# Kernel tuning notes

Measured on AMD Instinct MI355X. Metric: run time of the kernel, lower is better.

The kernel has to match this reference:

```python
import jax, jax.numpy as jnp
import numpy as np


def setup_inputs() -> dict:
    key = jax.random.key(0)
    k1, k2 = jax.random.split(key)
    T, K, D = 100000, 512, 64
    flags_matrix = jax.random.uniform(k1, (T, K), dtype=jnp.float32)  # ~half > 0.5
    emb_weight = jax.random.normal(k2, (K, D), dtype=jnp.float32)
    return {"flags_matrix": flags_matrix, "emb_weight": emb_weight}


def reference(flags_matrix, emb_weight):
    # mask[t,k] = 1 if flag active; bag-of-embeddings mean over active items per row.
    mask = (flags_matrix > 0.5).astype(emb_weight.dtype)          # [T, K]
    counts = jnp.sum(mask, axis=1, keepdims=True)                  # [T, 1]
    sums = mask @ emb_weight                                       # [T, D] masked sum of embeddings
    # rows with no active flags -> zeros (matches the torch branch)
    return jnp.where(counts > 0, sums / jnp.maximum(counts, 1.0), 0.0)
```

## Files before the change

### kernel.cpp

```cpp
#include <hip/hip_runtime.h>
#include <stdint.h>


#define T_ROWS 100000
#define K_FLAGS 512
#define D_DIM 64
#define TILES (T_ROWS / 16)

typedef __attribute__((ext_vector_type(4))) float f32x4;
typedef __attribute__((ext_vector_type(8))) short bf16x8;

__device__ __forceinline__ uint32_t f32_to_bf16_rne(float f) {
  union { float f; uint32_t u; } v; v.f = f;
  uint32_t u = v.u;
  return (u + 0x7FFFu + ((u >> 16) & 1u)) >> 16;
}

__global__ __launch_bounds__(1024, 8) void flagbag_kernel(const float* __restrict__ flags,
                                                          const float* __restrict__ W,
                                                          float* __restrict__ out) {
  __shared__ uint4 sB[16 * 4 * 64];
  __shared__ uint32_t sM[16][256];

  const int tid  = threadIdx.x;
  const int lane = tid & 63;
  const int wave = tid >> 6;
  const int tile = wave * 512 + (int)blockIdx.x;
  const bool active = (tile < TILES);
  const int t0 = (active ? tile : 0) * 16;

  if (active) {
    const float* ft = flags + (size_t)t0 * K_FLAGS + lane * 8;

    uint32_t D0 = 0, D1 = 0, D2 = 0, D3 = 0;
    f32x4 ra[4], rb[4];
#pragma unroll
    for (int r = 0; r < 3; ++r) {
      ra[r] = *reinterpret_cast<const f32x4*>(ft + r * K_FLAGS);
      rb[r] = *reinterpret_cast<const f32x4*>(ft + r * K_FLAGS + 4);
    }
#pragma unroll
    for (int r = 0; r < 16; ++r) {
      if (r + 3 < 16) {
        ra[(r + 3) & 3] = *reinterpret_cast<const f32x4*>(ft + (r + 3) * K_FLAGS);
        rb[(r + 3) & 3] = *reinterpret_cast<const f32x4*>(ft + (r + 3) * K_FLAGS + 4);
      }
      const f32x4 a = ra[r & 3], b = rb[r & 3];
      uint32_t byte = 0;
#pragma unroll
      for (int j = 0; j < 4; ++j) {
        byte |= (a[j] > 0.5f) ? (1u << j)       : 0u;
        byte |= (b[j] > 0.5f) ? (1u << (j + 4)) : 0u;
      }
      const uint32_t sh = byte << ((r & 3) * 8);
      if ((r >> 2) == 0) D0 |= sh;
      else if ((r >> 2) == 1) D1 |= sh;
      else if ((r >> 2) == 2) D2 |= sh;
      else D3 |= sh;
    }

    uint32_t* sMw = sM[wave];
    sMw[0 * 64 + (lane ^ 0)]  = D0;
    sMw[1 * 64 + (lane ^ 4)]  = D1;
    sMw[2 * 64 + (lane ^ 8)]  = D2;
    sMw[3 * 64 + (lane ^ 12)] = D3;
  }

  if (tid < 32) {
    const int e = tid >> 1, h = tid & 1;
    const uint32_t d = (((e >> (2 * h)) & 1)     ? 0x00003F80u : 0u) |
                       (((e >> (2 * h + 1)) & 1) ? 0x3F800000u : 0u);
    sM[15][e * 2 + h] = d;
  }

#pragma unroll
  for (int p = 0; p < 4; ++p) {
    const int E  = tid + p * 1024;
    const int s  = E >> 8;
    const int nt = (E >> 6) & 3;
    const int ln = E & 63;
    const int n  = (ln & 15) + 16 * nt;
    const int kb = 128 * (ln >> 4) + 8 * s;
    uint32_t r[4];
#pragma unroll
    for (int j = 0; j < 4; ++j) {
      uint32_t lo = f32_to_bf16_rne(W[(size_t)(kb + 2 * j    ) * D_DIM + n]);
      uint32_t hi = f32_to_bf16_rne(W[(size_t)(kb + 2 * j + 1) * D_DIM + n]);
      r[j] = lo | (hi << 16);
    }
    sB[E] = make_uint4(r[0], r[1], r[2], r[3]);
  }
  __syncthreads();
  if (!active) return;

  const int m  = lane & 15;
  const int kq = lane >> 4;
  const int mj = m >> 2, mb = m & 3;
  const uint32_t* sMw = sM[wave];
  const uint32_t* lut = sM[15];

  const uint4* sbl = &sB[lane];
  f32x4 acc[4];
#pragma unroll
  for (int nt = 0; nt < 4; ++nt) acc[nt] = (f32x4){0.f, 0.f, 0.f, 0.f};

  uint4 bc[4], bn[4];
#pragma unroll
  for (int nt = 0; nt < 4; ++nt) bc[nt] = sbl[nt * 64];

  int cnt = 0;
#pragma unroll
  for (int g = 0; g < 4; ++g) {
    const uint4 md = *reinterpret_cast<const uint4*>(&sMw[mj * 64 + 16 * kq + 4 * (g ^ mj)]);

#pragma unroll
    for (int q = 0; q < 4; ++q) {
      const int s = 4 * g + q;
      if (s + 1 < 16) {
#pragma unroll
        for (int nt = 0; nt < 4; ++nt) bn[nt] = sbl[((s + 1) * 4 + nt) * 64];
      }
      const uint32_t dw = (q == 0) ? md.x : (q == 1) ? md.y : (q == 2) ? md.z : md.w;
      const uint32_t byte = (dw >> (8 * mb)) & 0xFFu;
      cnt += __popc(byte);

      union { uint32_t d[4]; bf16x8 v; } af;
      const uint2 lo = *reinterpret_cast<const uint2*>(&lut[(byte & 15u) * 2]);
      const uint2 hi = *reinterpret_cast<const uint2*>(&lut[(byte >> 4) * 2]);
      af.d[0] = lo.x; af.d[1] = lo.y; af.d[2] = hi.x; af.d[3] = hi.y;

#pragma unroll
      for (int nt = 0; nt < 4; ++nt)
        acc[nt] = __builtin_amdgcn_mfma_f32_16x16x32_bf16(
            *reinterpret_cast<const bf16x8*>(&bc[nt]), af.v, acc[nt], 0, 0, 0);

#pragma unroll
      for (int nt = 0; nt < 4; ++nt) bc[nt] = bn[nt];
    }
  }

  cnt += __shfl_xor(cnt, 16);
  cnt += __shfl_xor(cnt, 32);
  const float inv = (cnt > 0) ? (1.0f / (float)cnt) : 0.0f;

  float* obase = out + (size_t)(t0 + m) * D_DIM + 4 * kq;
#pragma unroll
  for (int nt = 0; nt < 4; ++nt) {
    f32x4 v;
#pragma unroll
    for (int r = 0; r < 4; ++r) v[r] = acc[nt][r] * inv;
    *reinterpret_cast<f32x4*>(obase + 16 * nt) = v;
  }
}

extern "C" void kernel_launch(void* const* d_in, const int* in_sizes, int n_in,
                              void* d_out, int out_size, void* d_ws, size_t ws_size,
                              hipStream_t stream) {
  const float* flags = (const float*)d_in[0];
  const float* W     = (const float*)d_in[1];
  float* out         = (float*)d_out;

  hipLaunchKernelGGL(flagbag_kernel, dim3(512), dim3(1024), 0, stream, flags, W, out);
}
```

Before: 41.34 us.

## Switch to 32x32x16 MFMA with wave pairs sharing 32-row tiles

Each pair of waves now handles a 32-row tile, and each wave computes half of the 64 output columns using 32x32x16 bf16 MFMAs instead of four 16x16x32 MFMAs per step. Two accumulators alternate across k-steps so that consecutive dependent MFMAs are split, and they are summed at the end. The shared-memory B layout and the mask-byte addressing are rewritten to match the new operand layout. This reduces the number of MFMA issues and B-fragment LDS loads per row. In exchange it adds a per-step byte LDS read, and each wave now depends on its mate wave's mask data.

```diff
diff --git a/kernel.cpp b/kernel.cpp
--- a/kernel.cpp
+++ b/kernel.cpp
@@ -5,10 +5,11 @@
 #define T_ROWS 100000
 #define K_FLAGS 512
 #define D_DIM 64
-#define TILES (T_ROWS / 16)
+#define PAIRS (T_ROWS / 32)
 
-typedef __attribute__((ext_vector_type(4))) float f32x4;
-typedef __attribute__((ext_vector_type(8))) short bf16x8;
+typedef __attribute__((ext_vector_type(4)))  float f32x4;
+typedef __attribute__((ext_vector_type(16))) float f32x16;
+typedef __attribute__((ext_vector_type(8)))  short bf16x8;
 
 __device__ __forceinline__ uint32_t f32_to_bf16_rne(float f) {
   union { float f; uint32_t u; } v; v.f = f;
@@ -19,15 +20,17 @@
 __global__ __launch_bounds__(1024, 8) void flagbag_kernel(const float* __restrict__ flags,
                                                           const float* __restrict__ W,
                                                           float* __restrict__ out) {
-  __shared__ uint4 sB[16 * 4 * 64];
+  __shared__ uint4 sB[32 * 2 * 64];
   __shared__ uint32_t sM[16][256];
 
   const int tid  = threadIdx.x;
   const int lane = tid & 63;
   const int wave = tid >> 6;
-  const int tile = wave * 512 + (int)blockIdx.x;
-  const bool active = (tile < TILES);
-  const int t0 = (active ? tile : 0) * 16;
+  const int mate = wave & 1;
+  const int pair = (wave >> 1) * 512 + (int)blockIdx.x;
+  const bool active = (pair < PAIRS);
+  const int pb = (active ? pair : 0) * 32;
+  const int t0 = pb + 16 * mate;
 
   if (active) {
     const float* ft = flags + (size_t)t0 * K_FLAGS + lane * 8;
@@ -76,11 +79,11 @@
 #pragma unroll
   for (int p = 0; p < 4; ++p) {
     const int E  = tid + p * 1024;
-    const int s  = E >> 8;
-    const int nt = (E >> 6) & 3;
+    const int s  = E >> 7;
+    const int nt = (E >> 6) & 1;
     const int ln = E & 63;
-    const int n  = (ln & 15) + 16 * nt;
-    const int kb = 128 * (ln >> 4) + 8 * s;
+    const int n  = (ln & 31) + 32 * nt;
+    const int kb = 16 * s + 8 * (ln >> 5);
     uint32_t r[4];
 #pragma unroll
     for (int j = 0; j < 4; ++j) {
@@ -93,63 +96,52 @@
   __syncthreads();
   if (!active) return;
 
-  const int m  = lane & 15;
-  const int kq = lane >> 4;
-  const int mj = m >> 2, mb = m & 3;
-  const uint32_t* sMw = sM[wave];
+  const int trow = lane & 31;
+  const int kg   = lane >> 5;
+  const int lr   = trow & 15;
+  const int mj   = lr >> 2, mb = lr & 3, m2 = 2 * mj;
+  const uint8_t* sMs = reinterpret_cast<const uint8_t*>(sM[(wave & ~1) + (trow >> 4)]);
   const uint32_t* lut = sM[15];
 
-  const uint4* sbl = &sB[lane];
-  f32x4 acc[4];
+  f32x16 accA, accB;
 #pragma unroll
-  for (int nt = 0; nt < 4; ++nt) acc[nt] = (f32x4){0.f, 0.f, 0.f, 0.f};
+  for (int i = 0; i < 16; ++i) { accA[i] = 0.f; accB[i] = 0.f; }
+  int cnt = 0;
 
-  uint4 bc[4], bn[4];
+  uint4 bc = sB[mate * 64 + lane];
 #pragma unroll
-  for (int nt = 0; nt < 4; ++nt) bc[nt] = sbl[nt * 64];
+  for (int s = 0; s < 32; ++s) {
+    uint4 bn;
+    if (s + 1 < 32) bn = sB[(s + 1) * 128 + mate * 64 + lane];
 
-  int cnt = 0;
-#pragma unroll
-  for (int g = 0; g < 4; ++g) {
-    const uint4 md = *reinterpret_cast<const uint4*>(&sMw[mj * 64 + 16 * kq + 4 * (g ^ mj)]);
+    const uint32_t byte = sMs[(size_t)(mj * 64 + 2 * (s ^ m2) + kg) * 4 + mb];
+    cnt += __popc(byte);
 
-#pragma unroll
-    for (int q = 0; q < 4; ++q) {
-      const int s = 4 * g + q;
-      if (s + 1 < 16) {
-#pragma unroll
-        for (int nt = 0; nt < 4; ++nt) bn[nt] = sbl[((s + 1) * 4 + nt) * 64];
-      }
-      const uint32_t dw = (q == 0) ? md.x : (q == 1) ? md.y : (q == 2) ? md.z : md.w;
-      const uint32_t byte = (dw >> (8 * mb)) & 0xFFu;
-      cnt += __popc(byte);
+    union { uint32_t d[4]; bf16x8 v; } af;
+    const uint2 lo = *reinterpret_cast<const uint2*>(&lut[(byte & 15u) * 2]);
+    const uint2 hi = *reinterpret_cast<const uint2*>(&lut[(byte >> 4) * 2]);
+    af.d[0] = lo.x; af.d[1] = lo.y; af.d[2] = hi.x; af.d[3] = hi.y;
 
-      union { uint32_t d[4]; bf16x8 v; } af;
-      const uint2 lo = *reinterpret_cast<const uint2*>(&lut[(byte & 15u) * 2]);
-      const uint2 hi = *reinterpret_cast<const uint2*>(&lut[(byte >> 4) * 2]);
-      af.d[0] = lo.x; af.d[1] = lo.y; af.d[2] = hi.x; af.d[3] = hi.y;
+    if (s & 1)
+      accB = __builtin_amdgcn_mfma_f32_32x32x16_bf16(
+          *reinterpret_cast<const bf16x8*>(&bc), af.v, accB, 0, 0, 0);
+    else
+      accA = __builtin_amdgcn_mfma_f32_32x32x16_bf16(
+          *reinterpret_cast<const bf16x8*>(&bc), af.v, accA, 0, 0, 0);
 
-#pragma unroll
-      for (int nt = 0; nt < 4; ++nt)
-        acc[nt] = __builtin_amdgcn_mfma_f32_16x16x32_bf16(
-            *reinterpret_cast<const bf16x8*>(&bc[nt]), af.v, acc[nt], 0, 0, 0);
-
-#pragma unroll
-      for (int nt = 0; nt < 4; ++nt) bc[nt] = bn[nt];
-    }
+    bc = bn;
   }
 
-  cnt += __shfl_xor(cnt, 16);
   cnt += __shfl_xor(cnt, 32);
   const float inv = (cnt > 0) ? (1.0f / (float)cnt) : 0.0f;
 
-  float* obase = out + (size_t)(t0 + m) * D_DIM + 4 * kq;
+  float* obase = out + (size_t)(pb + trow) * D_DIM + 32 * mate + 4 * kg;
 #pragma unroll
-  for (int nt = 0; nt < 4; ++nt) {
+  for (int g = 0; g < 4; ++g) {
     f32x4 v;
 #pragma unroll
-    for (int r = 0; r < 4; ++r) v[r] = acc[nt][r] * inv;
-    *reinterpret_cast<f32x4*>(obase + 16 * nt) = v;
+    for (int r = 0; r < 4; ++r) v[r] = (accA[g * 4 + r] + accB[g * 4 + r]) * inv;
+    *reinterpret_cast<f32x4*>(obase + 8 * g) = v;
   }
 }
 
```

Measured after the change: 43.29 us. +4.7%, slower.
